# Kernel optimization log

Hardware: AMD Instinct MI355X
Metric: run time of the kernel (lower is better)

## Reference

```python
import jax, jax.numpy as jnp
import numpy as np

B, S, D, H = 32, 512, 512, 512  # batch, seq_len, input_size, hidden_size


def setup_inputs() -> dict:
    key = jax.random.key(0)
    ks = jax.random.split(key, 16)
    k = 1.0 / np.sqrt(H)  # torch LSTMCell init range
    def u(kk, shape):
        return jax.random.uniform(kk, shape, jnp.float32, -k, k)
    inp = {"x": jax.random.normal(ks[0], (B, S, D), jnp.float32)}
    # layer 0 cells consume D; layer 1 cells consume 2H (bidirectional concat)
    specs = [("f0", D), ("b0", D), ("f1", 2 * H), ("b1", 2 * H)]
    i = 1
    for name, din in specs:
        inp[f"Wih_{name}"] = u(ks[i], (4 * H, din)); i += 1
        inp[f"Whh_{name}"] = u(ks[i], (4 * H, H)); i += 1
        inp[f"b_{name}"] = u(ks[i], (4 * H,)); i += 1  # b_ih + b_hh folded into one bias
    return inp


def _run_dir(x, Wih, Whh, b, reverse):
    """One direction of one layer. x: [B, S, Din] -> (outputs [B, S, H], h_N, c_N)."""
    bsz = x.shape[0]
    xs = jnp.swapaxes(x, 0, 1)               # [S, B, Din]
    gx = xs @ Wih.T + b                      # precompute input projections [S, B, 4H]

    def step(carry, g_in):
        h, c = carry
        g = g_in + h @ Whh.T                 # [B, 4H]
        i_g, f_g, g_g, o_g = jnp.split(g, 4, axis=-1)  # torch gate order i,f,g,o
        c = jax.nn.sigmoid(f_g) * c + jax.nn.sigmoid(i_g) * jnp.tanh(g_g)
        h = jax.nn.sigmoid(o_g) * jnp.tanh(c)
        return (h, c), h

    h0 = jnp.zeros((bsz, H), x.dtype)
    c0 = jnp.zeros_like(h0)
    (hN, cN), ys = jax.lax.scan(step, (h0, c0), gx, reverse=reverse)
    return jnp.swapaxes(ys, 0, 1), hN, cN    # ys returned in original time order


def reference(x, Wih_f0, Whh_f0, b_f0, Wih_b0, Whh_b0, b_b0,
              Wih_f1, Whh_f1, b_f1, Wih_b1, Whh_b1, b_b1):
    layers = [((Wih_f0, Whh_f0, b_f0), (Wih_b0, Whh_b0, b_b0)),
              ((Wih_f1, Whh_f1, b_f1), (Wih_b1, Whh_b1, b_b1))]
    out = x
    for pf, pb in layers:
        fwd_out, h_f, c_f = _run_dir(out, *pf, reverse=False)
        bwd_out, h_b, c_b = _run_dir(out, *pb, reverse=True)
        out = jnp.concatenate([fwd_out, bwd_out], axis=-1)  # [B, S, 2H]
    h_n = jnp.stack([h_f, h_b], axis=0)
    c_n = jnp.stack([c_f, c_b], axis=0)
    return out, (h_n, c_n)
```

## Files before the change

### kernel.cpp

```cpp
#include <hip/hip_runtime.h>
#include <cstdint>
#include <cstddef>

#define BB 32
#define SS 512
#define HH 512
#define NBD 64
#define JPB 8
#define WR 32
#define WST 520

typedef short v8s __attribute__((ext_vector_type(8)));
typedef float v4f __attribute__((ext_vector_type(4)));
typedef unsigned long long u64t;

static __device__ __forceinline__ float b2f(unsigned short u) {
    union { unsigned int i; float f; } v; v.i = ((unsigned int)u) << 16; return v.f;
}
static __device__ __forceinline__ unsigned short f2b(float f) {
    union { float f; unsigned int i; } v; v.f = f;
    unsigned int u = v.i;
    return (unsigned short)((u + 0x7fffu + ((u >> 16) & 1u)) >> 16);
}
static __device__ __forceinline__ void split1(float f, short& hi, short& lo) {
    const unsigned short h = f2b(f);
    hi = (short)h;
    lo = (short)f2b(f - b2f(h));
}

#define MFMA(a, b, c) __builtin_amdgcn_mfma_f32_16x16x32_bf16((a), (b), (c), 0, 0, 0)

template<int DIN, bool L0>
__global__ __launch_bounds__(256, 1)
void lstm_layer(const void*  __restrict__ xin_,
                const float* __restrict__ Wih_f,
                const float* __restrict__ Whh_f,
                const float* __restrict__ b_f,
                const float* __restrict__ Wih_b,
                const float* __restrict__ Whh_b,
                const float* __restrict__ b_b,
                void*  __restrict__ yout_,
                u64t*  __restrict__ hrec,
                unsigned int* __restrict__ flags,
                float* __restrict__ hn,
                float* __restrict__ cn)
{
    constexpr int NKX = DIN / 32;
    constexpr int NKH = HH / 32;
    constexpr int XST = DIN + 8;

    extern __shared__ char smem[];
    unsigned short* WhhHi = (unsigned short*)smem;
    unsigned short* WihHi = WhhHi + WR * WST;
    unsigned short* hHi   = WihHi + WR * XST;

    const int tid   = threadIdx.x;
    const int dir   = blockIdx.x >> 6;
    const int jb    = blockIdx.x & 63;
    const int jbase = jb * JPB;

    const float* Wih = dir ? Wih_b : Wih_f;
    const float* Whh = dir ? Whh_b : Whh_f;
    const float* bv  = dir ? b_b  : b_f;

    {
        const int r = tid >> 3;
        const int R = (r & 3) * HH + jbase + (r >> 2);
        {
            const int c0 = (tid & 7) * 64;
            const float* src = Whh + (size_t)R * HH + c0;
            #pragma unroll
            for (int c = 0; c < 64; c += 8) {
                v8s hi;
                #pragma unroll
                for (int e = 0; e < 8; ++e) hi[e] = (short)f2b(src[c + e]);
                *(v8s*)(WhhHi + r * WST + c0 + c) = hi;
            }
        }
        {
            const int c0 = (tid & 7) * (DIN / 8);
            const float* src = Wih + (size_t)R * DIN + c0;
            #pragma unroll
            for (int c = 0; c < DIN / 8; c += 8) {
                v8s hi;
                #pragma unroll
                for (int e = 0; e < 8; ++e) hi[e] = (short)f2b(src[c + e]);
                *(v8s*)(WihHi + r * XST + c0 + c) = hi;
            }
        }
    }

    const int lane = tid & 63;
    const int wv   = tid >> 6;
    const int mi   = wv & 1;
    const int ni   = wv >> 1;
    const int g    = lane >> 4;
    const int rA   = lane & 15;

    const int brow = mi * 16 + rA;
    const int col  = ni * 16 + rA;
    const int jl   = col >> 2;
    const int p    = rA & 3;

    const float bi_ = bv[0 * HH + jbase + jl];
    const float bf_ = bv[1 * HH + jbase + jl];
    const float bg_ = bv[2 * HH + jbase + jl];
    const float bo_ = bv[3 * HH + jbase + jl];

    __syncthreads();

    const float*          aXf = L0 ? (const float*)xin_ + (size_t)brow * SS * DIN + 8 * g : nullptr;
    const unsigned short* aXb = L0 ? nullptr : (const unsigned short*)xin_ + (size_t)brow * SS * DIN + 8 * g;
    const unsigned short* bHh = WhhHi + col * WST + 8 * g;
    const unsigned short* bHx = WihHi + col * XST + 8 * g;

    unsigned int* fbase = flags + (size_t)dir * SS * 64;

    const int batch = mi * 16 + 4 * g + p;
    const int q  = tid & 127;
    const int k0 = tid >> 7;
    const int prodjb = q >> 1;
    float creg = 0.f;

    for (int st = 0; st < SS; ++st) {
        const int t = dir ? (SS - 1 - st) : st;

        v4f acc0 = {0,0,0,0}, acc1 = {0,0,0,0};
        v4f acc4 = {0,0,0,0}, acc5 = {0,0,0,0};

        if (L0) {
            const float* aX = aXf + (size_t)t * DIN;
            #pragma unroll
            for (int kt = 0; kt < NKX; kt += 2) {
                v8s ah0, al0, ah1, al1;
                #pragma unroll
                for (int e = 0; e < 8; ++e) {
                    short h, l;
                    split1(aX[kt * 32 + e], h, l);       ah0[e] = h; al0[e] = l;
                    split1(aX[(kt + 1) * 32 + e], h, l); ah1[e] = h; al1[e] = l;
                }
                v8s wh0 = *(const v8s*)(bHx + kt * 32);
                v8s wh1 = *(const v8s*)(bHx + (kt + 1) * 32);
                acc0 = MFMA(ah0, wh0, acc0);
                acc1 = MFMA(ah1, wh1, acc1);
                acc4 = MFMA(al0, wh0, acc4);
                acc5 = MFMA(al1, wh1, acc5);
            }
        } else {
            const unsigned short* aX = aXb + (size_t)t * DIN;
            #pragma unroll
            for (int kt = 0; kt < NKX; kt += 2) {
                v8s a0 = *(const v8s*)(aX + kt * 32);
                v8s a1 = *(const v8s*)(aX + (kt + 1) * 32);
                v8s wh0 = *(const v8s*)(bHx + kt * 32);
                v8s wh1 = *(const v8s*)(bHx + (kt + 1) * 32);
                acc0 = MFMA(a0, wh0, acc0);
                acc1 = MFMA(a1, wh1, acc1);
            }
        }

        if (st > 0) {
            {
                const unsigned int* f = fbase + (size_t)(st - 1) * 64 + prodjb;
                int guard = 0;
                while (!__hip_atomic_load(f, __ATOMIC_RELAXED,
                                          __HIP_MEMORY_SCOPE_AGENT)) {
                    __builtin_amdgcn_s_sleep(1);
                    if (++guard > (1 << 26)) break;
                }
            }
            const u64t* hsrc = hrec + (size_t)(dir * 2 + ((st - 1) & 1)) * (BB * HH / 4);
            u64t vals[16];
            #pragma unroll
            for (int i = 0; i < 16; ++i)
                vals[i] = __hip_atomic_load(hsrc + ((size_t)(k0 + 2 * i) * (HH / 4)) + q,
                                            __ATOMIC_RELAXED, __HIP_MEMORY_SCOPE_AGENT);
            #pragma unroll
            for (int i = 0; i < 16; ++i)
                *(u64t*)(hHi + (k0 + 2 * i) * WST + 4 * q) = vals[i];
            __syncthreads();

            const unsigned short* aHh = hHi + brow * WST + 8 * g;
            #pragma unroll
            for (int kt = 0; kt < NKH; kt += 2) {
                v8s ah0 = *(const v8s*)(aHh + kt * 32);
                v8s ah1 = *(const v8s*)(aHh + (kt + 1) * 32);
                v8s bh0 = *(const v8s*)(bHh + kt * 32);
                v8s bh1 = *(const v8s*)(bHh + (kt + 1) * 32);
                acc0 = MFMA(ah0, bh0, acc0);
                acc1 = MFMA(ah1, bh1, acc1);
            }
        }
        acc0 = acc0 + acc1;
        if (L0) acc0 += (acc4 + acc5);

        float pi_, pf_, pg_, po_;
        {
            const float x0 = acc0[0], x1 = acc0[1], x2 = acc0[2], x3 = acc0[3];
            const float n0 = __shfl_xor(x0, 1), n1 = __shfl_xor(x1, 1);
            const float n2 = __shfl_xor(x2, 1), n3 = __shfl_xor(x3, 1);
            const float a0 = (p & 1) ? n1 : x0;
            const float a1 = (p & 1) ? x1 : n0;
            const float a2 = (p & 1) ? n3 : x2;
            const float a3 = (p & 1) ? x3 : n2;
            const float m0 = __shfl_xor(a0, 2), m1 = __shfl_xor(a1, 2);
            const float m2 = __shfl_xor(a2, 2), m3 = __shfl_xor(a3, 2);
            pi_ = (p & 2) ? m2 : a0;
            pf_ = (p & 2) ? m3 : a1;
            pg_ = (p & 2) ? a2 : m0;
            po_ = (p & 2) ? a3 : m1;
        }

        {
            const float ig = 1.f / (1.f + __expf(-(pi_ + bi_)));
            const float fg = 1.f / (1.f + __expf(-(pf_ + bf_)));
            const float gg = tanhf(pg_ + bg_);
            const float og = 1.f / (1.f + __expf(-(po_ + bo_)));
            creg = fg * creg + ig * gg;
            const float h = og * tanhf(creg);
            const float hq1 = __shfl_xor(h, 4);
            const float hq2 = __shfl_xor(h, 8);
            const float hq3 = __shfl_xor(hq1, 8);

            if ((jl & 3) == 0) {
                const u64t pk = (u64t)f2b(h)
                              | ((u64t)f2b(hq1) << 16)
                              | ((u64t)f2b(hq2) << 32)
                              | ((u64t)f2b(hq3) << 48);
                u64t* hw = hrec + (size_t)(dir * 2 + (st & 1)) * (BB * HH / 4)
                         + (size_t)batch * (HH / 4) + ((jbase + jl) >> 2);
                __hip_atomic_store(hw, pk, __ATOMIC_RELAXED, __HIP_MEMORY_SCOPE_AGENT);
            }
            asm volatile("s_waitcnt vmcnt(0)" ::: "memory");
            __syncthreads();
            if (tid == 0)
                __hip_atomic_store(fbase + (size_t)st * 64 + jb, 1u,
                                   __ATOMIC_RELAXED, __HIP_MEMORY_SCOPE_AGENT);

            if (L0) {
                if ((jl & 1) == 0) {
                    const unsigned int pko = (unsigned int)f2b(h)
                                           | ((unsigned int)f2b(hq1) << 16);
                    *((unsigned int*)yout_ + (size_t)batch * SS * HH + (size_t)t * HH
                                           + dir * (HH / 2) + ((jbase + jl) >> 1)) = pko;
                }
            } else {
                ((float*)yout_)[((size_t)batch * SS + t) * (2 * HH) + dir * HH + jbase + jl] = h;
                if (st == SS - 1) {
                    hn[(dir * BB + batch) * HH + jbase + jl] = h;
                    cn[(dir * BB + batch) * HH + jbase + jl] = creg;
                }
            }
        }
    }
}

extern "C" void kernel_launch(void* const* d_in, const int* in_sizes, int n_in,
                              void* d_out, int out_size, void* d_ws, size_t ws_size,
                              hipStream_t stream) {
    (void)in_sizes; (void)n_in;

    const float* x      = (const float*)d_in[0];
    const float* Wih_f0 = (const float*)d_in[1];
    const float* Whh_f0 = (const float*)d_in[2];
    const float* b_f0   = (const float*)d_in[3];
    const float* Wih_b0 = (const float*)d_in[4];
    const float* Whh_b0 = (const float*)d_in[5];
    const float* b_b0   = (const float*)d_in[6];
    const float* Wih_f1 = (const float*)d_in[7];
    const float* Whh_f1 = (const float*)d_in[8];
    const float* b_f1   = (const float*)d_in[9];
    const float* Wih_b1 = (const float*)d_in[10];
    const float* Whh_b1 = (const float*)d_in[11];
    const float* b_b1   = (const float*)d_in[12];

    char* ws = (char*)d_ws;
    const size_t Y0B  = (size_t)BB * SS * 2 * HH * 2;
    const size_t FLG  = (size_t)2 * SS * 64 * 4;
    const size_t HREC = (size_t)2 * 2 * BB * (HH / 4) * 8;
    const size_t NEED = Y0B + 2 * FLG + HREC;
    if (ws_size < NEED) return;
    if ((size_t)out_size < (size_t)BB * SS * 2 * HH + 4 * BB * HH) return;

    unsigned short* y0     = (unsigned short*)(ws);
    unsigned int*   flags0 = (unsigned int*)(ws + Y0B);
    unsigned int*   flags1 = (unsigned int*)(ws + Y0B + FLG);
    u64t*           hrec   = (u64t*)(ws + Y0B + 2 * FLG);

    float* out = (float*)d_out;
    float* hn  = out + (size_t)BB * SS * 2 * HH;
    float* cn  = hn + 2 * BB * HH;

    hipMemsetAsync(ws + Y0B, 0, 2 * FLG, stream);

    constexpr int SMB0 = WR * WST * 2 + WR * (512 + 8) * 2 + BB * WST * 2;
    constexpr int SMB1 = WR * WST * 2 + WR * (1024 + 8) * 2 + BB * WST * 2;
    hipFuncSetAttribute(reinterpret_cast<const void*>(lstm_layer<512,  true>),
                        hipFuncAttributeMaxDynamicSharedMemorySize, SMB0);
    hipFuncSetAttribute(reinterpret_cast<const void*>(lstm_layer<1024, false>),
                        hipFuncAttributeMaxDynamicSharedMemorySize, SMB1);

    lstm_layer<512, true><<<128, 256, SMB0, stream>>>(
        x, Wih_f0, Whh_f0, b_f0, Wih_b0, Whh_b0, b_b0,
        (void*)y0, hrec, flags0, nullptr, nullptr);

    lstm_layer<1024, false><<<128, 256, SMB1, stream>>>(
        y0, Wih_f1, Whh_f1, b_f1, Wih_b1, Whh_b1, b_b1,
        (void*)out, hrec, flags1, hn, cn);
}
```

Measured before the change: 6.275 ms.

## Exchange recurrent hidden state through output buffer instead of separate ring buffer

Result: slower. 6.493 ms (+3.5%).

```diff
diff --git a/kernel.cpp b/kernel.cpp
--- a/kernel.cpp
+++ b/kernel.cpp
@@ -12,6 +12,7 @@
 
 typedef short v8s __attribute__((ext_vector_type(8)));
 typedef float v4f __attribute__((ext_vector_type(4)));
+typedef unsigned int v4u __attribute__((ext_vector_type(4)));
 typedef unsigned long long u64t;
 
 static __device__ __forceinline__ float b2f(unsigned short u) {
@@ -40,7 +41,6 @@
                 const float* __restrict__ Whh_b,
                 const float* __restrict__ b_b,
                 void*  __restrict__ yout_,
-                u64t*  __restrict__ hrec,
                 unsigned int* __restrict__ flags,
                 float* __restrict__ hn,
                 float* __restrict__ cn)
@@ -117,9 +117,6 @@
     unsigned int* fbase = flags + (size_t)dir * SS * 64;
 
     const int batch = mi * 16 + 4 * g + p;
-    const int q  = tid & 127;
-    const int k0 = tid >> 7;
-    const int prodjb = q >> 1;
     float creg = 0.f;
 
     for (int st = 0; st < SS; ++st) {
@@ -160,8 +157,9 @@
         }
 
         if (st > 0) {
-            {
-                const unsigned int* f = fbase + (size_t)(st - 1) * 64 + prodjb;
+            const int tp = dir ? t + 1 : t - 1;
+            if (tid < 64) {
+                const unsigned int* f = fbase + (size_t)(st - 1) * 64 + tid;
                 int guard = 0;
                 while (!__hip_atomic_load(f, __ATOMIC_RELAXED,
                                           __HIP_MEMORY_SCOPE_AGENT)) {
@@ -169,15 +167,34 @@
                     if (++guard > (1 << 26)) break;
                 }
             }
-            const u64t* hsrc = hrec + (size_t)(dir * 2 + ((st - 1) & 1)) * (BB * HH / 4);
-            u64t vals[16];
-            #pragma unroll
-            for (int i = 0; i < 16; ++i)
-                vals[i] = __hip_atomic_load(hsrc + ((size_t)(k0 + 2 * i) * (HH / 4)) + q,
-                                            __ATOMIC_RELAXED, __HIP_MEMORY_SCOPE_AGENT);
-            #pragma unroll
-            for (int i = 0; i < 16; ++i)
-                *(u64t*)(hHi + (k0 + 2 * i) * WST + 4 * q) = vals[i];
+            __syncthreads();
+
+            if (L0) {
+                const int c16 = tid & 63;
+                const int r0s = tid >> 6;
+                const char* yb = (const char*)yout_;
+                #pragma unroll
+                for (int i = 0; i < 8; ++i) {
+                    const int k = r0s + 4 * i;
+                    const v4u* s = (const v4u*)(yb
+                        + (((size_t)k * SS + tp) * (2 * HH) + dir * HH) * 2 + c16 * 16);
+                    *(v4u*)(hHi + k * WST + c16 * 8) = *s;
+                }
+            } else {
+                const int c   = tid & 127;
+                const int r0s = tid >> 7;
+                const float* yb = (const float*)yout_;
+                #pragma unroll
+                for (int i = 0; i < 16; ++i) {
+                    const int k = r0s + 2 * i;
+                    v4f v = *(const v4f*)(yb
+                        + ((size_t)k * SS + tp) * (2 * HH) + dir * HH + c * 4);
+                    const unsigned u0 = (unsigned)f2b(v[0]) | ((unsigned)f2b(v[1]) << 16);
+                    const unsigned u1 = (unsigned)f2b(v[2]) | ((unsigned)f2b(v[3]) << 16);
+                    const u64t pk = (u64t)u0 | ((u64t)u1 << 32);
+                    *(u64t*)(hHi + k * WST + c * 4) = pk;
+                }
+            }
             __syncthreads();
 
             const unsigned short* aHh = hHi + brow * WST + 8 * g;
@@ -219,17 +236,29 @@
             creg = fg * creg + ig * gg;
             const float h = og * tanhf(creg);
             const float hq1 = __shfl_xor(h, 4);
-            const float hq2 = __shfl_xor(h, 8);
-            const float hq3 = __shfl_xor(hq1, 8);
-
-            if ((jl & 3) == 0) {
-                const u64t pk = (u64t)f2b(h)
-                              | ((u64t)f2b(hq1) << 16)
-                              | ((u64t)f2b(hq2) << 32)
-                              | ((u64t)f2b(hq3) << 48);
-                u64t* hw = hrec + (size_t)(dir * 2 + (st & 1)) * (BB * HH / 4)
-                         + (size_t)batch * (HH / 4) + ((jbase + jl) >> 2);
-                __hip_atomic_store(hw, pk, __ATOMIC_RELAXED, __HIP_MEMORY_SCOPE_AGENT);
+
+            if (L0) {
+                const float hq2 = __shfl_xor(h, 8);
+                const float hq3 = __shfl_xor(hq1, 8);
+                if ((jl & 3) == 0) {
+                    const u64t pk = (u64t)f2b(h)
+                                  | ((u64t)f2b(hq1) << 16)
+                                  | ((u64t)f2b(hq2) << 32)
+                                  | ((u64t)f2b(hq3) << 48);
+                    unsigned short* yrow = (unsigned short*)yout_
+                        + ((size_t)batch * SS + t) * (2 * HH) + dir * HH + jbase + jl;
+                    __hip_atomic_store((u64t*)yrow, pk, __ATOMIC_RELAXED,
+                                       __HIP_MEMORY_SCOPE_AGENT);
+                }
+            } else {
+                if ((jl & 1) == 0) {
+                    const u64t pk = (u64t)__float_as_uint(h)
+                                  | ((u64t)__float_as_uint(hq1) << 32);
+                    float* yrow = (float*)yout_
+                        + ((size_t)batch * SS + t) * (2 * HH) + dir * HH + jbase + jl;
+                    __hip_atomic_store((u64t*)yrow, pk, __ATOMIC_RELAXED,
+                                       __HIP_MEMORY_SCOPE_AGENT);
+                }
             }
             asm volatile("s_waitcnt vmcnt(0)" ::: "memory");
             __syncthreads();
@@ -237,19 +266,9 @@
                 __hip_atomic_store(fbase + (size_t)st * 64 + jb, 1u,
                                    __ATOMIC_RELAXED, __HIP_MEMORY_SCOPE_AGENT);
 
-            if (L0) {
-                if ((jl & 1) == 0) {
-                    const unsigned int pko = (unsigned int)f2b(h)
-                                           | ((unsigned int)f2b(hq1) << 16);
-                    *((unsigned int*)yout_ + (size_t)batch * SS * HH + (size_t)t * HH
-                                           + dir * (HH / 2) + ((jbase + jl) >> 1)) = pko;
-                }
-            } else {
-                ((float*)yout_)[((size_t)batch * SS + t) * (2 * HH) + dir * HH + jbase + jl] = h;
-                if (st == SS - 1) {
-                    hn[(dir * BB + batch) * HH + jbase + jl] = h;
-                    cn[(dir * BB + batch) * HH + jbase + jl] = creg;
-                }
+            if (!L0 && st == SS - 1) {
+                hn[(dir * BB + batch) * HH + jbase + jl] = h;
+                cn[(dir * BB + batch) * HH + jbase + jl] = creg;
             }
         }
     }
@@ -277,15 +296,13 @@
     char* ws = (char*)d_ws;
     const size_t Y0B  = (size_t)BB * SS * 2 * HH * 2;
     const size_t FLG  = (size_t)2 * SS * 64 * 4;
-    const size_t HREC = (size_t)2 * 2 * BB * (HH / 4) * 8;
-    const size_t NEED = Y0B + 2 * FLG + HREC;
+    const size_t NEED = Y0B + 2 * FLG;
     if (ws_size < NEED) return;
     if ((size_t)out_size < (size_t)BB * SS * 2 * HH + 4 * BB * HH) return;
 
     unsigned short* y0     = (unsigned short*)(ws);
     unsigned int*   flags0 = (unsigned int*)(ws + Y0B);
     unsigned int*   flags1 = (unsigned int*)(ws + Y0B + FLG);
-    u64t*           hrec   = (u64t*)(ws + Y0B + 2 * FLG);
 
     float* out = (float*)d_out;
     float* hn  = out + (size_t)BB * SS * 2 * HH;
@@ -302,9 +319,9 @@
 
     lstm_layer<512, true><<<128, 256, SMB0, stream>>>(
         x, Wih_f0, Whh_f0, b_f0, Wih_b0, Whh_b0, b_b0,
-        (void*)y0, hrec, flags0, nullptr, nullptr);
+        (void*)y0, flags0, nullptr, nullptr);
 
     lstm_layer<1024, false><<<128, 256, SMB1, stream>>>(
         y0, Wih_f1, Whh_f1, b_f1, Wih_b1, Whh_b1, b_b1,
-        (void*)out, hrec, flags1, hn, cn);
-}
+        (void*)out, flags1, hn, cn);
+}
```
